# Optimization experiments

Hardware: AMD Instinct MI355X
Metric: run time of the kernel (lower is better)

The kernel has to match this reference:

```python
import jax, jax.numpy as jnp
import numpy as np

CE_SLICES = [(1,10),(12,29),(30,33),(33,40),(40,64),(64,79),(79,84),(84,94),(94,96),(96,99),(99,105),(105,113),(116,122),(122,128),(128,151),(151,159),(160,165)]
MSE_COLS = [0,10,11,29,113,114,115,159,165,166,167]
BINS = 800
RATIO_JSD = 0.1  # stand-in for par.RATIO_JSD (not defined in source)
B = 262144


def setup_inputs() -> dict:
    key = jax.random.key(0)
    k1, k2, k3, k4 = jax.random.split(key, 4)
    data_encoded = jax.random.normal(k1, (B, 11), dtype=jnp.float32)
    data_decoded = jax.random.normal(k2, (B, 168), dtype=jnp.float32)
    data_true = jax.random.normal(k3, (B, 168), dtype=jnp.float32)
    # categorical blocks of data_true must be one-hot (nonzero-based decode)
    for j, (s, e) in enumerate(CE_SLICES):
        lab = jax.random.randint(jax.random.fold_in(k3, j), (B,), 0, e - s)
        data_true = data_true.at[:, s:e].set(jax.nn.one_hot(lab, e - s, dtype=jnp.float32))
    label_true = jax.random.randint(k4, (B, 1), 0, 2).astype(jnp.float32)
    return {"data_encoded": data_encoded, "data_decoded": data_decoded,
            "data_true": data_true, "label_true": label_true, "batch_size": B}


def _ce(logits, labels):
    # F.cross_entropy with mean reduction
    logp = jax.nn.log_softmax(logits, axis=-1)
    return -jnp.mean(jnp.take_along_axis(logp, labels[:, None], axis=1))


def _hist(x, mn, mx, mask):
    # torch.histc semantics: BINS equal bins on [mn, mx], top edge inclusive.
    t = (x - mn) / (mx - mn)
    idx = jnp.clip(jnp.floor(t * BINS).astype(jnp.int32), 0, BINS - 1)
    return jax.ops.segment_sum(mask, idx, num_segments=BINS)


def _kl(p, q, eps=1e-12):
    return jnp.sum(jnp.where(p > 0, p * jnp.log((p + eps) / (q + eps)), 0.0))


def reference(data_encoded, data_decoded, data_true, label_true, batch_size):
    # ---- MSE losses over 11 scalar columns (vectorized) ----
    cols = jnp.array(MSE_COLS)
    diff = data_decoded[:, cols] - data_true[:, cols]            # [B, 11]
    mse_loss = jnp.sum(jnp.mean(diff * diff, axis=0))

    # ---- 17 cross-entropy heads (labels decoded from one-hot blocks) ----
    ce_loss = jnp.float32(0.0)
    for s, e in CE_SLICES:
        labels = jnp.argmax(data_true[:, s:e], axis=1)           # == first nonzero for one-hot
        ce_loss = ce_loss + _ce(data_decoded[:, s:e], labels)

    # ---- JSD between male/female histograms of first 10 encoded dims ----
    combined = jnp.concatenate([data_encoded, label_true], axis=1)  # [B, 12]
    mn = jnp.min(combined, axis=0)
    mx = jnp.max(combined, axis=0)
    male = (combined[:, 11] == 0).astype(jnp.float32)
    female = (combined[:, 11] == 1).astype(jnp.float32)
    cols10 = combined[:, :10].T                                  # [10, B]
    hist = jax.vmap(_hist, in_axes=(0, 0, 0, None))              # [10, BINS]
    m_h = hist(cols10, mn[:10], mx[:10], male) / jnp.sum(male)
    f_h = hist(cols10, mn[:10], mx[:10], female) / jnp.sum(female)
    mid = 0.5 * (m_h + f_h)
    kld = 0.5 * (_kl(m_h, mid) + _kl(f_h, mid))                  # Jensen-Shannon divergence

    multi = (1.0 - RATIO_JSD) * (mse_loss + ce_loss) + RATIO_JSD * kld
    return jnp.stack([multi, mse_loss, ce_loss, RATIO_JSD * kld])
```

## Files before the change

kernel.cpp:

```cpp
#include <hip/hip_runtime.h>
#include <math.h>


#define BINS 800
#define NHCOLS 10
#define HB_MAX 512

#define MIN_OFF 0
#define MAX_OFF 16
#define CNT_OFF 32
#define SUM_OFF 34
#define MH_OFF  64
#define FH_OFF  8064
#define PART_OFF 16384
#define WS_INIT_U32 64

__device__ __forceinline__ unsigned f2ord(float f) {
  unsigned u = __float_as_uint(f);
  return (u & 0x80000000u) ? ~u : (u | 0x80000000u);
}
__device__ __forceinline__ float ord2f(unsigned e) {
  return __uint_as_float((e & 0x80000000u) ? (e & 0x7FFFFFFFu) : ~e);
}

__global__ void k_init(unsigned* __restrict__ ws) {
  int i = blockIdx.x * blockDim.x + threadIdx.x;
  if (i < WS_INIT_U32) ws[i] = (i < 11) ? 0xFFFFFFFFu : 0u;
}

__global__ __launch_bounds__(256) void k_minmax(const float* __restrict__ enc,
                                                const float* __restrict__ lab,
                                                unsigned* __restrict__ ws, int B) {
  const int tid    = blockIdx.x * blockDim.x + threadIdx.x;
  const int stride = gridDim.x * blockDim.x;
  const int c      = tid % 11;
  unsigned mn = 0xFFFFFFFFu, mx = 0u;
  const long long total = (long long)B * 11;
  for (long long i = tid; i < total; i += stride) {
    unsigned e = f2ord(enc[i]);
    mn = mn < e ? mn : e;
    mx = mx > e ? mx : e;
  }
  __shared__ unsigned smn[11], smx[11], scnt[2];
  if (threadIdx.x < 11) { smn[threadIdx.x] = 0xFFFFFFFFu; smx[threadIdx.x] = 0u; }
  if (threadIdx.x < 2)  scnt[threadIdx.x] = 0u;
  __syncthreads();
  atomicMin(&smn[c], mn);
  atomicMax(&smx[c], mx);
  unsigned m = 0, f = 0;
  for (int i = tid; i < B; i += stride) {
    float v = lab[i];
    m += (v == 0.0f);
    f += (v == 1.0f);
  }
  atomicAdd(&scnt[0], m);
  atomicAdd(&scnt[1], f);
  __syncthreads();
  if (threadIdx.x < 11) {
    atomicMin(&ws[MIN_OFF + threadIdx.x], smn[threadIdx.x]);
    atomicMax(&ws[MAX_OFF + threadIdx.x], smx[threadIdx.x]);
  }
  if (threadIdx.x == 11) atomicAdd(&ws[CNT_OFF + 0], scnt[0]);
  if (threadIdx.x == 12) atomicAdd(&ws[CNT_OFF + 1], scnt[1]);
}

__global__ __launch_bounds__(256) void k_hist(const float* __restrict__ enc,
                                              const float* __restrict__ lab,
                                              unsigned* __restrict__ ws, int B, int hb) {
  __shared__ unsigned h[2][NHCOLS * BINS];
  __shared__ float smn[NHCOLS], srng[NHCOLS];
  unsigned* hf = &h[0][0];
  for (int i = threadIdx.x; i < 2 * NHCOLS * BINS; i += blockDim.x) hf[i] = 0u;
  if (threadIdx.x < NHCOLS) {
    float lo = ord2f(ws[MIN_OFF + threadIdx.x]);
    float hi = ord2f(ws[MAX_OFF + threadIdx.x]);
    smn[threadIdx.x] = lo;
    srng[threadIdx.x] = hi - lo;
  }
  __syncthreads();
  const int sub = (threadIdx.x >> 6) & 1;
  const int total  = B * 11;
  const int stride = hb << 8;
  for (int i = (blockIdx.x << 8) + threadIdx.x; i < total; i += stride) {
    const int r = i / 11;
    const int c = i - r * 11;
    if (c < NHCOLS) {
      float lv = lab[r];
      unsigned add = (lv == 0.0f) ? 1u : ((lv == 1.0f) ? 0x10000u : 0u);
      if (add) {
        float t = (enc[i] - smn[c]) / srng[c];
        int b = (int)floorf(t * 800.0f);
        b = b < 0 ? 0 : (b > BINS - 1 ? BINS - 1 : b);
        atomicAdd(&h[sub][c * BINS + b], add);
      }
    }
  }
  __syncthreads();
  for (int i = threadIdx.x; i < NHCOLS * BINS; i += blockDim.x)
    ws[PART_OFF + (size_t)blockIdx.x * (NHCOLS * BINS) + i] = h[0][i] + h[1][i];
}

__global__ __launch_bounds__(256) void k_merge(unsigned* __restrict__ ws, int hb) {
  int i = blockIdx.x * blockDim.x + threadIdx.x;
  if (i >= NHCOLS * BINS) return;
  unsigned m = 0, f = 0;
  const unsigned* p = ws + PART_OFF + i;
  for (int q = 0; q < hb; ++q) {
    unsigned v = p[(size_t)q * (NHCOLS * BINS)];
    m += v & 0xFFFFu;
    f += v >> 16;
  }
  ws[MH_OFF + i] = m;
  ws[FH_OFF + i] = f;
}

__host__ __device__ constexpr int slice_of(int c) {
  return (c>=1&&c<10)?0:(c>=12&&c<29)?1:(c>=30&&c<33)?2:(c>=33&&c<40)?3:
         (c>=40&&c<64)?4:(c>=64&&c<79)?5:(c>=79&&c<84)?6:(c>=84&&c<94)?7:
         (c>=94&&c<96)?8:(c>=96&&c<99)?9:(c>=99&&c<105)?10:(c>=105&&c<113)?11:
         (c>=116&&c<122)?12:(c>=122&&c<128)?13:(c>=128&&c<151)?14:
         (c>=151&&c<159)?15:(c>=160&&c<165)?16:-1;
}
__host__ __device__ constexpr bool mse_of(int c) {
  return c==0||c==10||c==11||c==29||c==113||c==114||c==115||c==159||
         c==165||c==166||c==167;
}

template<int I, int K>
__device__ __forceinline__ void elem(const float (&d)[11][4], const float (&t)[11][4],
                                     float (&s)[17], float &dot, float &mse, int j) {
  constexpr int c0 = 16*I + K, c1 = c0+4, c2 = c0+8, c3 = c0+12;
  constexpr int cem = ((c0<168 && slice_of(c0)>=0)?1:0) |
                      ((c1<168 && slice_of(c1)>=0)?2:0) |
                      ((c2<168 && slice_of(c2)>=0)?4:0) |
                      ((c3<168 && slice_of(c3)>=0)?8:0);
  constexpr int msm = ((c0<168 && mse_of(c0))?1:0) | ((c1<168 && mse_of(c1))?2:0) |
                      ((c2<168 && mse_of(c2))?4:0) | ((c3<168 && mse_of(c3))?8:0);
  const float dv = d[I][K], tv = t[I][K];
  if constexpr (cem != 0) {
    float e = __expf(dv);
    if constexpr (cem & 1) s[slice_of(c0)] += (j == 0) ? e : 0.0f;
    if constexpr (cem & 2) s[slice_of(c1)] += (j == 1) ? e : 0.0f;
    if constexpr (cem & 4) s[slice_of(c2)] += (j == 2) ? e : 0.0f;
    if constexpr (cem & 8) s[slice_of(c3)] += (j == 3) ? e : 0.0f;
    dot += ((cem >> j) & 1) ? tv * dv : 0.0f;
  }
  if constexpr (msm != 0) {
    float df = dv - tv;
    mse += ((msm >> j) & 1) ? df * df : 0.0f;
  }
}

template<int I>
__device__ __forceinline__ void elem_row(const float (&d)[11][4], const float (&t)[11][4],
                                         float (&s)[17], float &dot, float &mse, int j) {
  elem<I,0>(d, t, s, dot, mse, j);
  elem<I,1>(d, t, s, dot, mse, j);
  elem<I,2>(d, t, s, dot, mse, j);
  elem<I,3>(d, t, s, dot, mse, j);
}

__global__ __launch_bounds__(256, 2) void k_main(const float* __restrict__ dec,
                                                 const float* __restrict__ tru,
                                                 float* __restrict__ wsf, int B) {
  const int lane = threadIdx.x & 63;
  const int wid  = threadIdx.x >> 6;
  const int j    = lane & 3;
  const int row  = blockIdx.x * 64 + (wid << 4) + (lane >> 2);
  const bool valid = row < B;
  const int rowc = valid ? row : (B - 1);

  float d[11][4], t[11][4];
  const float4* d4 = (const float4*)(dec + (size_t)rowc * 168);
  const float4* t4 = (const float4*)(tru + (size_t)rowc * 168);
#pragma unroll
  for (int i = 0; i < 11; ++i) {
    int w = 4 * i + j;
    w = w > 41 ? 41 : w;
    const float4 dv = d4[w];
    const float4 tv = t4[w];
    d[i][0] = dv.x; d[i][1] = dv.y; d[i][2] = dv.z; d[i][3] = dv.w;
    t[i][0] = tv.x; t[i][1] = tv.y; t[i][2] = tv.z; t[i][3] = tv.w;
  }
  __builtin_amdgcn_sched_barrier(0);

  float s[17];
#pragma unroll
  for (int k = 0; k < 17; ++k) s[k] = 0.0f;
  float dot = 0.0f, mse = 0.0f;

  elem_row<0>(d, t, s, dot, mse, j);
  elem_row<1>(d, t, s, dot, mse, j);
  elem_row<2>(d, t, s, dot, mse, j);
  elem_row<3>(d, t, s, dot, mse, j);
  elem_row<4>(d, t, s, dot, mse, j);
  elem_row<5>(d, t, s, dot, mse, j);
  elem_row<6>(d, t, s, dot, mse, j);
  elem_row<7>(d, t, s, dot, mse, j);
  elem_row<8>(d, t, s, dot, mse, j);
  elem_row<9>(d, t, s, dot, mse, j);
  elem_row<10>(d, t, s, dot, mse, j);

  dot += __shfl_xor(dot, 1, 64);
  dot += __shfl_xor(dot, 2, 64);
#pragma unroll
  for (int k = 0; k < 17; ++k) {
    s[k] += __shfl_xor(s[k], 1, 64);
    s[k] += __shfl_xor(s[k], 2, 64);
  }
  float ce = -dot;
#pragma unroll
  for (int k = 0; k < 17; ++k) ce += __logf(s[k]);

  ce  = (valid && j == 0) ? ce : 0.0f;
  mse = valid ? mse : 0.0f;

  __shared__ float sm[4], sc[4];
#pragma unroll
  for (int off = 32; off > 0; off >>= 1) {
    mse += __shfl_down(mse, off, 64);
    ce  += __shfl_down(ce, off, 64);
  }
  if (lane == 0) { sm[wid] = mse; sc[wid] = ce; }
  __syncthreads();
  if (threadIdx.x == 0) {
    atomicAdd(&wsf[SUM_OFF + 0], sm[0] + sm[1] + sm[2] + sm[3]);
    atomicAdd(&wsf[SUM_OFF + 1], sc[0] + sc[1] + sc[2] + sc[3]);
  }
}

__global__ __launch_bounds__(256) void k_final(const unsigned* __restrict__ ws,
                                               float* __restrict__ out, int B) {
  const float* wsf = (const float*)ws;
  float male   = (float)ws[CNT_OFF + 0];
  float female = (float)ws[CNT_OFF + 1];
  float local = 0.0f;
  for (int i = threadIdx.x; i < NHCOLS * BINS; i += blockDim.x) {
    float mh  = (float)ws[MH_OFF + i] / male;
    float fh  = (float)ws[FH_OFF + i] / female;
    float mid = 0.5f * (mh + fh);
    if (mh > 0.0f) local += mh * logf((mh + 1e-12f) / (mid + 1e-12f));
    if (fh > 0.0f) local += fh * logf((fh + 1e-12f) / (mid + 1e-12f));
  }
  __shared__ float s[4];
  int lane = threadIdx.x & 63, wid = threadIdx.x >> 6;
#pragma unroll
  for (int off = 32; off > 0; off >>= 1) local += __shfl_down(local, off, 64);
  if (lane == 0) s[wid] = local;
  __syncthreads();
  if (threadIdx.x == 0) {
    float kld   = 0.5f * (s[0] + s[1] + s[2] + s[3]);
    float mse   = wsf[SUM_OFF + 0] / (float)B;
    float ce    = wsf[SUM_OFF + 1] / (float)B;
    float multi = 0.9f * (mse + ce) + 0.1f * kld;
    out[0] = multi;
    out[1] = mse;
    out[2] = ce;
    out[3] = 0.1f * kld;
  }
}

extern "C" void kernel_launch(void* const* d_in, const int* in_sizes, int n_in,
                              void* d_out, int out_size, void* d_ws, size_t ws_size,
                              hipStream_t stream) {
  (void)n_in; (void)out_size;
  const float* enc = (const float*)d_in[0];
  const float* dec = (const float*)d_in[1];
  const float* tru = (const float*)d_in[2];
  const float* lab = (const float*)d_in[3];
  const int B = in_sizes[3];
  unsigned* ws = (unsigned*)d_ws;
  float* out = (float*)d_out;

  int hb = HB_MAX;
  {
    size_t avail = ws_size / 4;
    if (avail > (size_t)PART_OFF) {
      size_t cap = (avail - (size_t)PART_OFF) / (size_t)(NHCOLS * BINS);
      if ((size_t)hb > cap) hb = (int)cap;
    } else {
      hb = 1;
    }
    if (hb < 1) hb = 1;
  }

  hipLaunchKernelGGL(k_init, dim3(1), dim3(64), 0, stream, ws);
  hipLaunchKernelGGL(k_minmax, dim3(352), dim3(256), 0, stream, enc, lab, ws, B);
  hipLaunchKernelGGL(k_hist, dim3(hb), dim3(256), 0, stream, enc, lab, ws, B, hb);
  hipLaunchKernelGGL(k_merge, dim3((NHCOLS * BINS + 255) / 256), dim3(256), 0, stream, ws, hb);
  hipLaunchKernelGGL(k_main, dim3((B + 63) / 64), dim3(256), 0, stream,
                     dec, tru, (float*)ws, B);
  hipLaunchKernelGGL(k_final, dim3(1), dim3(256), 0, stream, ws, out, B);
}
```

Before: 514.0 us.

## Merge histogram partials via global atomics, spread loss atomics, raise k_main occupancy

The histogram kernel now runs a fixed 256 blocks and adds its per-block shared-memory histograms straight into the global male/female histograms with atomics. This removes the partial-histogram buffer and the separate merge kernel. The row/column index is advanced incrementally instead of divided each iteration. k_main now targets 3 waves per SIMD instead of 2, and the sched barrier is replaced by empty asm register pins. Its final MSE/CE atomics are spread over 64 padded slots that k_final reduces, which costs more workspace initialisation and adds contention on the global histogram atomics.

```diff
diff --git a/kernel.cpp b/kernel.cpp
--- a/kernel.cpp
+++ b/kernel.cpp
@@ -4,16 +4,16 @@
 
 #define BINS 800
 #define NHCOLS 10
-#define HB_MAX 512
+#define HBLK 256
 
 #define MIN_OFF 0
 #define MAX_OFF 16
 #define CNT_OFF 32
-#define SUM_OFF 34
 #define MH_OFF  64
 #define FH_OFF  8064
-#define PART_OFF 16384
-#define WS_INIT_U32 64
+#define SUM2_OFF 16384
+#define SUM2_CE  (SUM2_OFF + 2048)
+#define WS_TOTAL_U32 20480
 
 __device__ __forceinline__ unsigned f2ord(float f) {
   unsigned u = __float_as_uint(f);
@@ -25,7 +25,7 @@
 
 __global__ void k_init(unsigned* __restrict__ ws) {
   int i = blockIdx.x * blockDim.x + threadIdx.x;
-  if (i < WS_INIT_U32) ws[i] = (i < 11) ? 0xFFFFFFFFu : 0u;
+  if (i < WS_TOTAL_U32) ws[i] = (i < 11) ? 0xFFFFFFFFu : 0u;
 }
 
 __global__ __launch_bounds__(256) void k_minmax(const float* __restrict__ enc,
@@ -66,7 +66,7 @@
 
 __global__ __launch_bounds__(256) void k_hist(const float* __restrict__ enc,
                                               const float* __restrict__ lab,
-                                              unsigned* __restrict__ ws, int B, int hb) {
+                                              unsigned* __restrict__ ws, int B) {
   __shared__ unsigned h[2][NHCOLS * BINS];
   __shared__ float smn[NHCOLS], srng[NHCOLS];
   unsigned* hf = &h[0][0];
@@ -78,12 +78,15 @@
     srng[threadIdx.x] = hi - lo;
   }
   __syncthreads();
-  const int sub = (threadIdx.x >> 6) & 1;
+  const int sub    = (threadIdx.x >> 6) & 1;
   const int total  = B * 11;
-  const int stride = hb << 8;
-  for (int i = (blockIdx.x << 8) + threadIdx.x; i < total; i += stride) {
-    const int r = i / 11;
-    const int c = i - r * 11;
+  const int stride = HBLK * 256;
+  const int qs     = stride / 11;
+  const int rs     = stride % 11;
+  int i = blockIdx.x * 256 + threadIdx.x;
+  int r = i / 11;
+  int c = i - r * 11;
+  for (; i < total; i += stride) {
     if (c < NHCOLS) {
       float lv = lab[r];
       unsigned add = (lv == 0.0f) ? 1u : ((lv == 1.0f) ? 0x10000u : 0u);
@@ -94,24 +97,16 @@
         atomicAdd(&h[sub][c * BINS + b], add);
       }
     }
-  }
-  __syncthreads();
-  for (int i = threadIdx.x; i < NHCOLS * BINS; i += blockDim.x)
-    ws[PART_OFF + (size_t)blockIdx.x * (NHCOLS * BINS) + i] = h[0][i] + h[1][i];
-}
-
-__global__ __launch_bounds__(256) void k_merge(unsigned* __restrict__ ws, int hb) {
-  int i = blockIdx.x * blockDim.x + threadIdx.x;
-  if (i >= NHCOLS * BINS) return;
-  unsigned m = 0, f = 0;
-  const unsigned* p = ws + PART_OFF + i;
-  for (int q = 0; q < hb; ++q) {
-    unsigned v = p[(size_t)q * (NHCOLS * BINS)];
-    m += v & 0xFFFFu;
-    f += v >> 16;
-  }
-  ws[MH_OFF + i] = m;
-  ws[FH_OFF + i] = f;
+    r += qs; c += rs;
+    if (c >= 11) { c -= 11; ++r; }
+  }
+  __syncthreads();
+  for (int k = threadIdx.x; k < NHCOLS * BINS; k += blockDim.x) {
+    unsigned v = h[0][k] + h[1][k];
+    unsigned m = v & 0xFFFFu, f = v >> 16;
+    if (m) atomicAdd(&ws[MH_OFF + k], m);
+    if (f) atomicAdd(&ws[FH_OFF + k], f);
+  }
 }
 
 __host__ __device__ constexpr int slice_of(int c) {
@@ -160,7 +155,7 @@
   elem<I,3>(d, t, s, dot, mse, j);
 }
 
-__global__ __launch_bounds__(256, 2) void k_main(const float* __restrict__ dec,
+__global__ __launch_bounds__(256, 3) void k_main(const float* __restrict__ dec,
                                                  const float* __restrict__ tru,
                                                  float* __restrict__ wsf, int B) {
   const int lane = threadIdx.x & 63;
@@ -182,7 +177,11 @@
     d[i][0] = dv.x; d[i][1] = dv.y; d[i][2] = dv.z; d[i][3] = dv.w;
     t[i][0] = tv.x; t[i][1] = tv.y; t[i][2] = tv.z; t[i][3] = tv.w;
   }
-  __builtin_amdgcn_sched_barrier(0);
+#pragma unroll
+  for (int i = 0; i < 11; ++i) {
+    asm volatile("" : "+v"(d[i][0]), "+v"(d[i][1]), "+v"(d[i][2]), "+v"(d[i][3]),
+                      "+v"(t[i][0]), "+v"(t[i][1]), "+v"(t[i][2]), "+v"(t[i][3]));
+  }
 
   float s[17];
 #pragma unroll
@@ -224,8 +223,9 @@
   if (lane == 0) { sm[wid] = mse; sc[wid] = ce; }
   __syncthreads();
   if (threadIdx.x == 0) {
-    atomicAdd(&wsf[SUM_OFF + 0], sm[0] + sm[1] + sm[2] + sm[3]);
-    atomicAdd(&wsf[SUM_OFF + 1], sc[0] + sc[1] + sc[2] + sc[3]);
+    const int slot = (blockIdx.x & 63) * 32;
+    atomicAdd(&wsf[SUM2_OFF + slot], sm[0] + sm[1] + sm[2] + sm[3]);
+    atomicAdd(&wsf[SUM2_CE  + slot], sc[0] + sc[1] + sc[2] + sc[3]);
   }
 }
 
@@ -242,16 +242,26 @@
     if (mh > 0.0f) local += mh * logf((mh + 1e-12f) / (mid + 1e-12f));
     if (fh > 0.0f) local += fh * logf((fh + 1e-12f) / (mid + 1e-12f));
   }
-  __shared__ float s[4];
   int lane = threadIdx.x & 63, wid = threadIdx.x >> 6;
-#pragma unroll
-  for (int off = 32; off > 0; off >>= 1) local += __shfl_down(local, off, 64);
+  float msep = 0.0f, cep = 0.0f;
+  if (threadIdx.x < 64) {
+    msep = wsf[SUM2_OFF + threadIdx.x * 32];
+    cep  = wsf[SUM2_CE  + threadIdx.x * 32];
+  }
+  __shared__ float s[4], sm2, sc2;
+#pragma unroll
+  for (int off = 32; off > 0; off >>= 1) {
+    local += __shfl_down(local, off, 64);
+    msep  += __shfl_down(msep, off, 64);
+    cep   += __shfl_down(cep, off, 64);
+  }
   if (lane == 0) s[wid] = local;
+  if (threadIdx.x == 0) { sm2 = msep; sc2 = cep; }
   __syncthreads();
   if (threadIdx.x == 0) {
     float kld   = 0.5f * (s[0] + s[1] + s[2] + s[3]);
-    float mse   = wsf[SUM_OFF + 0] / (float)B;
-    float ce    = wsf[SUM_OFF + 1] / (float)B;
+    float mse   = sm2 / (float)B;
+    float ce    = sc2 / (float)B;
     float multi = 0.9f * (mse + ce) + 0.1f * kld;
     out[0] = multi;
     out[1] = mse;
@@ -263,7 +273,7 @@
 extern "C" void kernel_launch(void* const* d_in, const int* in_sizes, int n_in,
                               void* d_out, int out_size, void* d_ws, size_t ws_size,
                               hipStream_t stream) {
-  (void)n_in; (void)out_size;
+  (void)n_in; (void)out_size; (void)ws_size;
   const float* enc = (const float*)d_in[0];
   const float* dec = (const float*)d_in[1];
   const float* tru = (const float*)d_in[2];
@@ -272,22 +282,9 @@
   unsigned* ws = (unsigned*)d_ws;
   float* out = (float*)d_out;
 
-  int hb = HB_MAX;
-  {
-    size_t avail = ws_size / 4;
-    if (avail > (size_t)PART_OFF) {
-      size_t cap = (avail - (size_t)PART_OFF) / (size_t)(NHCOLS * BINS);
-      if ((size_t)hb > cap) hb = (int)cap;
-    } else {
-      hb = 1;
-    }
-    if (hb < 1) hb = 1;
-  }
-
-  hipLaunchKernelGGL(k_init, dim3(1), dim3(64), 0, stream, ws);
+  hipLaunchKernelGGL(k_init, dim3((WS_TOTAL_U32 + 255) / 256), dim3(256), 0, stream, ws);
   hipLaunchKernelGGL(k_minmax, dim3(352), dim3(256), 0, stream, enc, lab, ws, B);
-  hipLaunchKernelGGL(k_hist, dim3(hb), dim3(256), 0, stream, enc, lab, ws, B, hb);
-  hipLaunchKernelGGL(k_merge, dim3((NHCOLS * BINS + 255) / 256), dim3(256), 0, stream, ws, hb);
+  hipLaunchKernelGGL(k_hist, dim3(HBLK), dim3(256), 0, stream, enc, lab, ws, B);
   hipLaunchKernelGGL(k_main, dim3((B + 63) / 64), dim3(256), 0, stream,
                      dec, tru, (float*)ws, B);
   hipLaunchKernelGGL(k_final, dim3(1), dim3(256), 0, stream, ws, out, B);
```

New measurement: 443.0 us. 1.16x faster.
